# Performance work log

Measured on AMD Instinct MI355X. Metric: run time of the kernel, lower is better.

The kernel has to match this reference:

```python
import jax, jax.numpy as jnp
import numpy as np

D_MODEL = 1024
NUM_HEADS = 16
D_HEAD = D_MODEL // NUM_HEADS
BATCH = 2
SEQ = 2048


def setup_inputs() -> dict:
    key = jax.random.key(0)
    ks = jax.random.split(key, 5)
    std = 0.02
    return {
        "x": jax.random.normal(ks[0], (BATCH, SEQ, D_MODEL), dtype=jnp.float32),
        "Wq": jax.random.normal(ks[1], (D_MODEL, D_MODEL), dtype=jnp.float32) * std,
        "Wk": jax.random.normal(ks[2], (D_MODEL, D_MODEL), dtype=jnp.float32) * std,
        "Wv": jax.random.normal(ks[3], (D_MODEL, D_MODEL), dtype=jnp.float32) * std,
        "Wo": jax.random.normal(ks[4], (D_MODEL, D_MODEL), dtype=jnp.float32) * std,
    }


def reference(x, Wq, Wk, Wv, Wo):
    batch, seq_len, d_model = x.shape
    h, dh = NUM_HEADS, D_HEAD

    def split_heads(W):
        # x @ W.T -> (b, s, d) -> (b, h, s, dh)
        p = jnp.einsum('bsd,ed->bse', x, W)
        return p.reshape(batch, seq_len, h, dh).transpose(0, 2, 1, 3)

    Q = split_heads(Wq)
    K = split_heads(Wk)
    V = split_heads(Wv)

    scale = 1.0 / jnp.sqrt(jnp.asarray(dh, dtype=x.dtype))
    scores = jnp.einsum('bhqd,bhkd->bhqk', Q, K) * scale
    causal = jnp.tril(jnp.ones((seq_len, seq_len), dtype=bool))
    scores = jnp.where(causal, scores, -jnp.inf)
    attn = jax.nn.softmax(scores, axis=-1)
    out = jnp.einsum('bhqk,bhkd->bhqd', attn, V)  # (b, h, s, dh)
    out = out.transpose(0, 2, 1, 3).reshape(batch, seq_len, d_model)
    return jnp.einsum('bsd,ed->bse', out, Wo)
```

## Files before the change

kernel.cpp:

```cpp
#include <hip/hip_runtime.h>

#define D_MODEL 1024
#define NUM_HEADS 16
#define D_HEAD 64
#define BATCH 2
#define SEQ 2048
#define MTOT (BATCH * SEQ)
#define PLANE ((size_t)MTOT * D_MODEL)
#define QSCALE 0.1803368801f

typedef unsigned short us;
typedef __bf16 bf16x8 __attribute__((ext_vector_type(8)));
typedef float floatx4 __attribute__((ext_vector_type(4)));

__device__ __forceinline__ unsigned int f2bf(float f) {
  union { float f; unsigned int i; } v; v.f = f;
  unsigned int r = v.i + 0x7FFFu + ((v.i >> 16) & 1u);
  return r >> 16;
}
__device__ __forceinline__ unsigned int f2bf_tr(float f) {
  union { float f; unsigned int i; } v; v.f = f;
  return v.i >> 16;
}

__global__ __launch_bounds__(256) void convert_all(const float* __restrict__ x,
                                                   const float* __restrict__ Wq,
                                                   const float* __restrict__ Wk,
                                                   const float* __restrict__ Wv,
                                                   us* __restrict__ xbf,
                                                   us* __restrict__ Wqkv) {
  const int i = blockIdx.x * 256 + threadIdx.x;
  const float* src;
  us* dst;
  if (i < (1 << 20)) {
    src = x + (size_t)i * 4;
    dst = xbf + (size_t)i * 4;
  } else {
    const int j = i - (1 << 20);
    const int w = j >> 18;
    const int o = j & ((1 << 18) - 1);
    const float* ws = (w == 0) ? Wq : (w == 1) ? Wk : Wv;
    src = ws + (size_t)o * 4;
    dst = Wqkv + (size_t)w * (D_MODEL * D_MODEL) + (size_t)o * 4;
  }
  float4 v = *(const float4*)src;
  uint2 pk;
  pk.x = f2bf(v.x) | (f2bf(v.y) << 16);
  pk.y = f2bf(v.z) | (f2bf(v.w) << 16);
  *(uint2*)dst = pk;
}

__global__ __launch_bounds__(256) void convert_bf16(const float* __restrict__ src,
                                                    us* __restrict__ dst, int n4) {
  int i = blockIdx.x * 256 + threadIdx.x;
  if (i >= n4) return;
  float4 v = *(const float4*)(src + (size_t)i * 4);
  uint2 pk;
  pk.x = f2bf(v.x) | (f2bf(v.y) << 16);
  pk.y = f2bf(v.z) | (f2bf(v.w) << 16);
  *(uint2*)(dst + (size_t)i * 4) = pk;
}

template <int CMODE>
__global__ __launch_bounds__(256) void gemm_mfma(const us* __restrict__ A,
                                                 const us* __restrict__ B,
                                                 void* __restrict__ Cv,
                                                 int M, int N, int K) {
  __shared__ __bf16 As[128 * 32];
  __shared__ __bf16 Bs[128 * 32];
  const int tid = threadIdx.x;
  const int wid = tid >> 6;
  const int lane = tid & 63;
  const int bm = blockIdx.y * 128;
  const int bn = blockIdx.x * 128;
  const int wm = (wid & 1) * 64;
  const int wn = (wid >> 1) * 64;
  const int lr = lane & 15;
  const int quad = lane >> 4;

  floatx4 acc[4][4] = {};
  const int cb0 = wid * 128;

  for (int k0 = 0; k0 < K; k0 += 32) {
    __syncthreads();
#pragma unroll
    for (int p = 0; p < 2; ++p) {
      const int cb = cb0 + p * 64;
      const int c = cb + lane;
      const us* ga = A + (size_t)(bm + (c >> 2)) * K + (k0 + (c & 3) * 8);
      const us* gb = B + (size_t)(bn + (c >> 2)) * K + (k0 + (c & 3) * 8);
      __builtin_amdgcn_global_load_lds((const __attribute__((address_space(1))) void*)ga,
                                       (__attribute__((address_space(3))) void*)(&As[cb * 8]),
                                       16, 0, 0);
      __builtin_amdgcn_global_load_lds((const __attribute__((address_space(1))) void*)gb,
                                       (__attribute__((address_space(3))) void*)(&Bs[cb * 8]),
                                       16, 0, 0);
    }
    __syncthreads();

    bf16x8 a[4], b[4];
#pragma unroll
    for (int i = 0; i < 4; ++i)
      a[i] = *(const bf16x8*)&As[(wm + i * 16 + lr) * 32 + quad * 8];
#pragma unroll
    for (int j = 0; j < 4; ++j)
      b[j] = *(const bf16x8*)&Bs[(wn + j * 16 + lr) * 32 + quad * 8];
#pragma unroll
    for (int i = 0; i < 4; ++i)
#pragma unroll
      for (int j = 0; j < 4; ++j)
        acc[i][j] = __builtin_amdgcn_mfma_f32_16x16x32_bf16(a[i], b[j], acc[i][j], 0, 0, 0);
  }

#pragma unroll
  for (int i = 0; i < 4; ++i) {
#pragma unroll
    for (int j = 0; j < 4; ++j) {
      const int col = bn + wn + j * 16 + lr;
      if constexpr (CMODE == 1) {
        us* dst = (us*)Cv;
        const int plane = col >> 10;
        if (plane < 2) {
          const float s = (plane == 0) ? QSCALE : 1.0f;
#pragma unroll
          for (int r = 0; r < 4; ++r) {
            const int row = bm + wm + i * 16 + quad * 4 + r;
            dst[(size_t)plane * PLANE + (size_t)row * 1024 + (col & 1023)] =
                (us)f2bf(acc[i][j][r] * s);
          }
        } else {
          const int d = col & 63;
          const int hh = (col >> 6) & 15;
          const int row0 = bm + wm + i * 16 + quad * 4;
          const int bb = row0 >> 11;
          const int ss = row0 & 2047;
          uint2 pk;
          pk.x = f2bf(acc[i][j][0]) | (f2bf(acc[i][j][1]) << 16);
          pk.y = f2bf(acc[i][j][2]) | (f2bf(acc[i][j][3]) << 16);
          *(uint2*)&dst[2 * PLANE + ((size_t)((bb * 16 + hh) * 64 + d)) * 2048 + ss] = pk;
        }
      } else {
#pragma unroll
        for (int r = 0; r < 4; ++r) {
          const int row = bm + wm + i * 16 + quad * 4 + r;
          ((float*)Cv)[(size_t)row * N + col] = acc[i][j][r];
        }
      }
    }
  }
}

#define ASTR 72

__global__ __launch_bounds__(512, 2) void attn_mfma(const us* __restrict__ Qb,
                                                    const us* __restrict__ Kb,
                                                    const us* __restrict__ Vtg,
                                                    us* __restrict__ Ob) {
  const int bx = blockIdx.x;
  const int b = bx >> 8;
  const int idx = bx & 255;
  const int h = idx >> 4;
  const int s0 = idx & 15;
  const int strip = b ? (15 - s0) : s0;
  const int q0 = strip * 128;
  const int ntiles = 2 * strip + 2;
  const int tid = threadIdx.x;
  const int w = tid >> 6;
  const int lane = tid & 63;
  const int lr = lane & 15;
  const int quad = lane >> 4;

  __shared__ us Ks[2][64 * ASTR];
  __shared__ us Vs[2][64 * ASTR];
  __shared__ us Ps[8 * 16 * ASTR];

  const us* kbase = Kb + (size_t)(b * SEQ) * D_MODEL + h * D_HEAD;
  const us* vbase = Vtg + (size_t)((b * 16 + h) * 64) * 2048;
  us* const pg = &Ps[w * 16 * ASTR];

  const int grow = q0 + w * 16;
  const us* qp = Qb + (size_t)(b * SEQ + grow + lr) * D_MODEL + h * D_HEAD;
  const bf16x8 qa0 = *(const bf16x8*)(qp + quad * 8);
  const bf16x8 qa1 = *(const bf16x8*)(qp + 32 + quad * 8);

  floatx4 oacc[4] = {};
  floatx4 lacc = {};
  bf16x8 ones;
#pragma unroll
  for (int i = 0; i < 8; ++i) ones[i] = (__bf16)1.0f;

  const int srow = tid >> 3;
  const int schunk = tid & 7;

  uint4 kreg, vreg;
  kreg = *(const uint4*)(kbase + (size_t)srow * D_MODEL + schunk * 8);
  vreg = *(const uint4*)(vbase + (size_t)srow * 2048 + schunk * 8);
  *(uint4*)&Ks[0][srow * ASTR + schunk * 8] = kreg;
  *(uint4*)&Vs[0][srow * ASTR + schunk * 8] = vreg;
  __syncthreads();

  for (int t = 0; t < ntiles; ++t) {
    const int k0 = t * 64;
    const int cur = t & 1;
    const bool more = (t + 1 < ntiles);

    if (more) {
      const int kn = k0 + 64;
      kreg = *(const uint4*)(kbase + (size_t)(kn + srow) * D_MODEL + schunk * 8);
      vreg = *(const uint4*)(vbase + (size_t)srow * 2048 + kn + schunk * 8);
    }

#pragma unroll
    for (int jt = 0; jt < 4; ++jt) {
      const bf16x8 kb0 = *(const bf16x8*)&Ks[cur][(jt * 16 + lr) * ASTR + quad * 8];
      const bf16x8 kb1 = *(const bf16x8*)&Ks[cur][(jt * 16 + lr) * ASTR + 32 + quad * 8];
      floatx4 s = {};
      s = __builtin_amdgcn_mfma_f32_16x16x32_bf16(kb0, qa0, s, 0, 0, 0);
      s = __builtin_amdgcn_mfma_f32_16x16x32_bf16(kb1, qa1, s, 0, 0, 0);
      const int kb = k0 + jt * 16 + quad * 4;
      const bool needMask = (k0 + jt * 16 + 15 > grow);
      float p[4];
#pragma unroll
      for (int r = 0; r < 4; ++r) {
        float e = __builtin_amdgcn_exp2f(s[r]);
        if (needMask && (kb + r > grow + lr)) e = 0.f;
        p[r] = e;
      }
      uint2 pk;
      pk.x = f2bf_tr(p[0]) | (f2bf_tr(p[1]) << 16);
      pk.y = f2bf_tr(p[2]) | (f2bf_tr(p[3]) << 16);
      *(uint2*)&pg[lr * ASTR + jt * 16 + quad * 4] = pk;
    }

    const bf16x8 pa0 = *(const bf16x8*)&pg[lr * ASTR + quad * 8];
    const bf16x8 pa1 = *(const bf16x8*)&pg[lr * ASTR + 32 + quad * 8];
    lacc = __builtin_amdgcn_mfma_f32_16x16x32_bf16(ones, pa0, lacc, 0, 0, 0);
    lacc = __builtin_amdgcn_mfma_f32_16x16x32_bf16(ones, pa1, lacc, 0, 0, 0);
#pragma unroll
    for (int nt = 0; nt < 4; ++nt) {
      const bf16x8 vb0 = *(const bf16x8*)&Vs[cur][(nt * 16 + lr) * ASTR + quad * 8];
      const bf16x8 vb1 = *(const bf16x8*)&Vs[cur][(nt * 16 + lr) * ASTR + 32 + quad * 8];
      oacc[nt] = __builtin_amdgcn_mfma_f32_16x16x32_bf16(vb0, pa0, oacc[nt], 0, 0, 0);
      oacc[nt] = __builtin_amdgcn_mfma_f32_16x16x32_bf16(vb1, pa1, oacc[nt], 0, 0, 0);
    }

    if (more) {
      const int nxt = cur ^ 1;
      *(uint4*)&Ks[nxt][srow * ASTR + schunk * 8] = kreg;
      *(uint4*)&Vs[nxt][srow * ASTR + schunk * 8] = vreg;
    }
    __syncthreads();
  }

  const float inv = 1.f / lacc[0];
#pragma unroll
  for (int nt = 0; nt < 4; ++nt) {
    uint2 pk;
    pk.x = f2bf_tr(oacc[nt][0] * inv) | (f2bf_tr(oacc[nt][1] * inv) << 16);
    pk.y = f2bf_tr(oacc[nt][2] * inv) | (f2bf_tr(oacc[nt][3] * inv) << 16);
    *(uint2*)&pg[lr * ASTR + nt * 16 + quad * 4] = pk;
  }
#pragma unroll
  for (int p = 0; p < 2; ++p) {
    const int c = lane + 64 * p;
    *(uint4*)(Ob + (size_t)(b * SEQ + grow + (c >> 3)) * D_MODEL + h * D_HEAD + (c & 7) * 8) =
        *(const uint4*)&pg[(c >> 3) * ASTR + (c & 7) * 8];
  }
}

extern "C" void kernel_launch(void* const* d_in, const int* in_sizes, int n_in,
                              void* d_out, int out_size, void* d_ws, size_t ws_size,
                              hipStream_t stream) {
  const float* x  = (const float*)d_in[0];
  const float* Wq = (const float*)d_in[1];
  const float* Wk = (const float*)d_in[2];
  const float* Wv = (const float*)d_in[3];
  const float* Wo = (const float*)d_in[4];

  us* xbf = (us*)d_ws;
  us* Qb  = xbf + PLANE;
  us* Kb  = xbf + 2 * PLANE;
  us* Vt  = xbf + 3 * PLANE;
  us* Ab  = xbf;
  us* Wqkv = (us*)d_out;
  us* Wobf = Qb;
  float* out = (float*)d_out;

  const int WN = D_MODEL * D_MODEL;

  convert_all<<<7168, 256, 0, stream>>>(x, Wq, Wk, Wv, xbf, Wqkv);

  gemm_mfma<1><<<dim3(3072 / 128, MTOT / 128), 256, 0, stream>>>(xbf, Wqkv, Qb, MTOT, 3072, D_MODEL);

  attn_mfma<<<512, 512, 0, stream>>>(Qb, Kb, Vt, Ab);

  convert_bf16<<<WN / 4 / 256, 256, 0, stream>>>(Wo, Wobf, WN / 4);
  gemm_mfma<2><<<dim3(D_MODEL / 128, MTOT / 128), 256, 0, stream>>>(Ab, Wobf, out, MTOT, D_MODEL, D_MODEL);
}
```

Baseline: 182.7 us.

## Read attention K/V straight from global memory, reorder blocks, fold Wo conversion

The attention kernel drops its double-buffered shared-memory K/V tiles and barriers. Each wave now loads its K and V MFMA operands directly from global memory and relies on the cache for reuse across the 8 waves. Blocks are reordered so the longest causal strips launch first across all batch/head pairs. The Wo bf16 conversion is merged into the initial conversion kernel, removing one launch, and its output moves to a separate workspace plane. The risk is extra global/L2 traffic and exposed load latency in the attention inner loop now that nothing prefetches.

```diff
diff --git a/kernel.cpp b/kernel.cpp
--- a/kernel.cpp
+++ b/kernel.cpp
@@ -27,8 +27,10 @@
                                                    const float* __restrict__ Wq,
                                                    const float* __restrict__ Wk,
                                                    const float* __restrict__ Wv,
+                                                   const float* __restrict__ Wo,
                                                    us* __restrict__ xbf,
-                                                   us* __restrict__ Wqkv) {
+                                                   us* __restrict__ Wqkv,
+                                                   us* __restrict__ Wobf) {
   const int i = blockIdx.x * 256 + threadIdx.x;
   const float* src;
   us* dst;
@@ -39,26 +41,20 @@
     const int j = i - (1 << 20);
     const int w = j >> 18;
     const int o = j & ((1 << 18) - 1);
-    const float* ws = (w == 0) ? Wq : (w == 1) ? Wk : Wv;
-    src = ws + (size_t)o * 4;
-    dst = Wqkv + (size_t)w * (D_MODEL * D_MODEL) + (size_t)o * 4;
+    if (w < 3) {
+      const float* ws = (w == 0) ? Wq : (w == 1) ? Wk : Wv;
+      src = ws + (size_t)o * 4;
+      dst = Wqkv + (size_t)w * (D_MODEL * D_MODEL) + (size_t)o * 4;
+    } else {
+      src = Wo + (size_t)o * 4;
+      dst = Wobf + (size_t)o * 4;
+    }
   }
   float4 v = *(const float4*)src;
   uint2 pk;
   pk.x = f2bf(v.x) | (f2bf(v.y) << 16);
   pk.y = f2bf(v.z) | (f2bf(v.w) << 16);
   *(uint2*)dst = pk;
-}
-
-__global__ __launch_bounds__(256) void convert_bf16(const float* __restrict__ src,
-                                                    us* __restrict__ dst, int n4) {
-  int i = blockIdx.x * 256 + threadIdx.x;
-  if (i >= n4) return;
-  float4 v = *(const float4*)(src + (size_t)i * 4);
-  uint2 pk;
-  pk.x = f2bf(v.x) | (f2bf(v.y) << 16);
-  pk.y = f2bf(v.z) | (f2bf(v.w) << 16);
-  *(uint2*)(dst + (size_t)i * 4) = pk;
 }
 
 template <int CMODE>
@@ -157,11 +153,10 @@
                                                     const us* __restrict__ Vtg,
                                                     us* __restrict__ Ob) {
   const int bx = blockIdx.x;
-  const int b = bx >> 8;
-  const int idx = bx & 255;
-  const int h = idx >> 4;
-  const int s0 = idx & 15;
-  const int strip = b ? (15 - s0) : s0;
+  const int strip = 15 - (bx >> 5);
+  const int bh = bx & 31;
+  const int b = bh >> 4;
+  const int h = bh & 15;
   const int q0 = strip * 128;
   const int ntiles = 2 * strip + 2;
   const int tid = threadIdx.x;
@@ -170,13 +165,11 @@
   const int lr = lane & 15;
   const int quad = lane >> 4;
 
-  __shared__ us Ks[2][64 * ASTR];
-  __shared__ us Vs[2][64 * ASTR];
   __shared__ us Ps[8 * 16 * ASTR];
+  us* const pg = &Ps[w * 16 * ASTR];
 
   const us* kbase = Kb + (size_t)(b * SEQ) * D_MODEL + h * D_HEAD;
   const us* vbase = Vtg + (size_t)((b * 16 + h) * 64) * 2048;
-  us* const pg = &Ps[w * 16 * ASTR];
 
   const int grow = q0 + w * 16;
   const us* qp = Qb + (size_t)(b * SEQ + grow + lr) * D_MODEL + h * D_HEAD;
@@ -189,31 +182,14 @@
 #pragma unroll
   for (int i = 0; i < 8; ++i) ones[i] = (__bf16)1.0f;
 
-  const int srow = tid >> 3;
-  const int schunk = tid & 7;
-
-  uint4 kreg, vreg;
-  kreg = *(const uint4*)(kbase + (size_t)srow * D_MODEL + schunk * 8);
-  vreg = *(const uint4*)(vbase + (size_t)srow * 2048 + schunk * 8);
-  *(uint4*)&Ks[0][srow * ASTR + schunk * 8] = kreg;
-  *(uint4*)&Vs[0][srow * ASTR + schunk * 8] = vreg;
-  __syncthreads();
-
   for (int t = 0; t < ntiles; ++t) {
     const int k0 = t * 64;
-    const int cur = t & 1;
-    const bool more = (t + 1 < ntiles);
-
-    if (more) {
-      const int kn = k0 + 64;
-      kreg = *(const uint4*)(kbase + (size_t)(kn + srow) * D_MODEL + schunk * 8);
-      vreg = *(const uint4*)(vbase + (size_t)srow * 2048 + kn + schunk * 8);
-    }
 
 #pragma unroll
     for (int jt = 0; jt < 4; ++jt) {
-      const bf16x8 kb0 = *(const bf16x8*)&Ks[cur][(jt * 16 + lr) * ASTR + quad * 8];
-      const bf16x8 kb1 = *(const bf16x8*)&Ks[cur][(jt * 16 + lr) * ASTR + 32 + quad * 8];
+      const us* krow = kbase + (size_t)(k0 + jt * 16 + lr) * D_MODEL;
+      const bf16x8 kb0 = *(const bf16x8*)(krow + quad * 8);
+      const bf16x8 kb1 = *(const bf16x8*)(krow + 32 + quad * 8);
       floatx4 s = {};
       s = __builtin_amdgcn_mfma_f32_16x16x32_bf16(kb0, qa0, s, 0, 0, 0);
       s = __builtin_amdgcn_mfma_f32_16x16x32_bf16(kb1, qa1, s, 0, 0, 0);
@@ -238,18 +214,12 @@
     lacc = __builtin_amdgcn_mfma_f32_16x16x32_bf16(ones, pa1, lacc, 0, 0, 0);
 #pragma unroll
     for (int nt = 0; nt < 4; ++nt) {
-      const bf16x8 vb0 = *(const bf16x8*)&Vs[cur][(nt * 16 + lr) * ASTR + quad * 8];
-      const bf16x8 vb1 = *(const bf16x8*)&Vs[cur][(nt * 16 + lr) * ASTR + 32 + quad * 8];
+      const us* vrow = vbase + (size_t)(nt * 16 + lr) * 2048 + k0;
+      const bf16x8 vb0 = *(const bf16x8*)(vrow + quad * 8);
+      const bf16x8 vb1 = *(const bf16x8*)(vrow + 32 + quad * 8);
       oacc[nt] = __builtin_amdgcn_mfma_f32_16x16x32_bf16(vb0, pa0, oacc[nt], 0, 0, 0);
       oacc[nt] = __builtin_amdgcn_mfma_f32_16x16x32_bf16(vb1, pa1, oacc[nt], 0, 0, 0);
     }
-
-    if (more) {
-      const int nxt = cur ^ 1;
-      *(uint4*)&Ks[nxt][srow * ASTR + schunk * 8] = kreg;
-      *(uint4*)&Vs[nxt][srow * ASTR + schunk * 8] = vreg;
-    }
-    __syncthreads();
   }
 
   const float inv = 1.f / lacc[0];
@@ -281,19 +251,16 @@
   us* Qb  = xbf + PLANE;
   us* Kb  = xbf + 2 * PLANE;
   us* Vt  = xbf + 3 * PLANE;
+  us* Wobf = xbf + 4 * PLANE;
   us* Ab  = xbf;
   us* Wqkv = (us*)d_out;
-  us* Wobf = Qb;
   float* out = (float*)d_out;
 
-  const int WN = D_MODEL * D_MODEL;
-
-  convert_all<<<7168, 256, 0, stream>>>(x, Wq, Wk, Wv, xbf, Wqkv);
+  convert_all<<<8192, 256, 0, stream>>>(x, Wq, Wk, Wv, Wo, xbf, Wqkv, Wobf);
 
   gemm_mfma<1><<<dim3(3072 / 128, MTOT / 128), 256, 0, stream>>>(xbf, Wqkv, Qb, MTOT, 3072, D_MODEL);
 
   attn_mfma<<<512, 512, 0, stream>>>(Qb, Kb, Vt, Ab);
 
-  convert_bf16<<<WN / 4 / 256, 256, 0, stream>>>(Wo, Wobf, WN / 4);
   gemm_mfma<2><<<dim3(D_MODEL / 128, MTOT / 128), 256, 0, stream>>>(Ab, Wobf, out, MTOT, D_MODEL, D_MODEL);
 }
```

Result: slower. 316.9 us (+73.4%).

## Double-buffer GEMM LDS tiles and fold Wo conversion into convert kernel

Applied to the files above, without the earlier changes.

The GEMM kernel now uses two LDS buffers so the next K-tile's global-to-LDS load is issued before the MFMA work on the current tile, with one barrier per iteration instead of two. The Wo fp32-to-bf16 conversion is merged into the initial convert kernel, removing a separate launch, and Wobf gets its own workspace region. This doubles LDS use per block and needs more workspace.

```diff
diff --git a/kernel.cpp b/kernel.cpp
--- a/kernel.cpp
+++ b/kernel.cpp
@@ -27,8 +27,10 @@
                                                    const float* __restrict__ Wq,
                                                    const float* __restrict__ Wk,
                                                    const float* __restrict__ Wv,
+                                                   const float* __restrict__ Wo,
                                                    us* __restrict__ xbf,
-                                                   us* __restrict__ Wqkv) {
+                                                   us* __restrict__ Wqkv,
+                                                   us* __restrict__ Wobf) {
   const int i = blockIdx.x * 256 + threadIdx.x;
   const float* src;
   us* dst;
@@ -39,9 +41,14 @@
     const int j = i - (1 << 20);
     const int w = j >> 18;
     const int o = j & ((1 << 18) - 1);
-    const float* ws = (w == 0) ? Wq : (w == 1) ? Wk : Wv;
-    src = ws + (size_t)o * 4;
-    dst = Wqkv + (size_t)w * (D_MODEL * D_MODEL) + (size_t)o * 4;
+    if (w < 3) {
+      const float* ws = (w == 0) ? Wq : (w == 1) ? Wk : Wv;
+      src = ws + (size_t)o * 4;
+      dst = Wqkv + (size_t)w * (D_MODEL * D_MODEL) + (size_t)o * 4;
+    } else {
+      src = Wo + (size_t)o * 4;
+      dst = Wobf + (size_t)o * 4;
+    }
   }
   float4 v = *(const float4*)src;
   uint2 pk;
@@ -50,24 +57,13 @@
   *(uint2*)dst = pk;
 }
 
-__global__ __launch_bounds__(256) void convert_bf16(const float* __restrict__ src,
-                                                    us* __restrict__ dst, int n4) {
-  int i = blockIdx.x * 256 + threadIdx.x;
-  if (i >= n4) return;
-  float4 v = *(const float4*)(src + (size_t)i * 4);
-  uint2 pk;
-  pk.x = f2bf(v.x) | (f2bf(v.y) << 16);
-  pk.y = f2bf(v.z) | (f2bf(v.w) << 16);
-  *(uint2*)(dst + (size_t)i * 4) = pk;
-}
-
 template <int CMODE>
 __global__ __launch_bounds__(256) void gemm_mfma(const us* __restrict__ A,
                                                  const us* __restrict__ B,
                                                  void* __restrict__ Cv,
                                                  int M, int N, int K) {
-  __shared__ __bf16 As[128 * 32];
-  __shared__ __bf16 Bs[128 * 32];
+  __shared__ __bf16 As[2][128 * 32];
+  __shared__ __bf16 Bs[2][128 * 32];
   const int tid = threadIdx.x;
   const int wid = tid >> 6;
   const int lane = tid & 63;
@@ -81,8 +77,7 @@
   floatx4 acc[4][4] = {};
   const int cb0 = wid * 128;
 
-  for (int k0 = 0; k0 < K; k0 += 32) {
-    __syncthreads();
+  auto stage = [&](int buf, int k0) {
 #pragma unroll
     for (int p = 0; p < 2; ++p) {
       const int cb = cb0 + p * 64;
@@ -90,26 +85,36 @@
       const us* ga = A + (size_t)(bm + (c >> 2)) * K + (k0 + (c & 3) * 8);
       const us* gb = B + (size_t)(bn + (c >> 2)) * K + (k0 + (c & 3) * 8);
       __builtin_amdgcn_global_load_lds((const __attribute__((address_space(1))) void*)ga,
-                                       (__attribute__((address_space(3))) void*)(&As[cb * 8]),
+                                       (__attribute__((address_space(3))) void*)(&As[buf][cb * 8]),
                                        16, 0, 0);
       __builtin_amdgcn_global_load_lds((const __attribute__((address_space(1))) void*)gb,
-                                       (__attribute__((address_space(3))) void*)(&Bs[cb * 8]),
+                                       (__attribute__((address_space(3))) void*)(&Bs[buf][cb * 8]),
                                        16, 0, 0);
     }
-    __syncthreads();
+  };
+
+  stage(0, 0);
+  __syncthreads();
+
+  int cur = 0;
+  for (int k0 = 0; k0 < K; k0 += 32) {
+    if (k0 + 32 < K) stage(cur ^ 1, k0 + 32);
 
     bf16x8 a[4], b[4];
 #pragma unroll
     for (int i = 0; i < 4; ++i)
-      a[i] = *(const bf16x8*)&As[(wm + i * 16 + lr) * 32 + quad * 8];
+      a[i] = *(const bf16x8*)&As[cur][(wm + i * 16 + lr) * 32 + quad * 8];
 #pragma unroll
     for (int j = 0; j < 4; ++j)
-      b[j] = *(const bf16x8*)&Bs[(wn + j * 16 + lr) * 32 + quad * 8];
+      b[j] = *(const bf16x8*)&Bs[cur][(wn + j * 16 + lr) * 32 + quad * 8];
 #pragma unroll
     for (int i = 0; i < 4; ++i)
 #pragma unroll
       for (int j = 0; j < 4; ++j)
         acc[i][j] = __builtin_amdgcn_mfma_f32_16x16x32_bf16(a[i], b[j], acc[i][j], 0, 0, 0);
+
+    __syncthreads();
+    cur ^= 1;
   }
 
 #pragma unroll
@@ -281,19 +286,16 @@
   us* Qb  = xbf + PLANE;
   us* Kb  = xbf + 2 * PLANE;
   us* Vt  = xbf + 3 * PLANE;
+  us* Wobf = xbf + 4 * PLANE;
   us* Ab  = xbf;
   us* Wqkv = (us*)d_out;
-  us* Wobf = Qb;
   float* out = (float*)d_out;
 
-  const int WN = D_MODEL * D_MODEL;
-
-  convert_all<<<7168, 256, 0, stream>>>(x, Wq, Wk, Wv, xbf, Wqkv);
+  convert_all<<<8192, 256, 0, stream>>>(x, Wq, Wk, Wv, Wo, xbf, Wqkv, Wobf);
 
   gemm_mfma<1><<<dim3(3072 / 128, MTOT / 128), 256, 0, stream>>>(xbf, Wqkv, Qb, MTOT, 3072, D_MODEL);
 
   attn_mfma<<<512, 512, 0, stream>>>(Qb, Kb, Vt, Ab);
 
-  convert_bf16<<<WN / 4 / 256, 256, 0, stream>>>(Wo, Wobf, WN / 4);
   gemm_mfma<2><<<dim3(D_MODEL / 128, MTOT / 128), 256, 0, stream>>>(Ab, Wobf, out, MTOT, D_MODEL, D_MODEL);
 }
```

Measured after the change: 175.7 us. 1.04x faster.
